# Kernel optimization log

Hardware: AMD Instinct MI355X
Metric: run time of the kernel (lower is better)

## Reference

```python
import jax, jax.numpy as jnp
import numpy as np

B, N, DIM = 4, 2048, 1024
HEADS, DIM_HEAD = 16, 64
INNER = HEADS * DIM_HEAD  # 1024
SCALE = DIM_HEAD ** -0.5

def setup_inputs() -> dict:
    key = jax.random.key(0)
    k1, k2, k3 = jax.random.split(key, 3)
    x = jax.random.normal(k1, (B, N, DIM), dtype=jnp.float32)
    w_qkv = jax.random.normal(k2, (DIM, 3 * INNER), dtype=jnp.float32) * (DIM ** -0.5)
    w_out = jax.random.normal(k3, (INNER, DIM), dtype=jnp.float32) * (INNER ** -0.5)
    b_out = jnp.zeros((DIM,), dtype=jnp.float32)
    return {"x": x, "w_qkv": w_qkv, "w_out": w_out, "b_out": b_out}

def reference(x, w_qkv, w_out, b_out):
    b, n, _ = x.shape
    qkv = x @ w_qkv  # [b, n, 3*inner]
    q, k, v = jnp.split(qkv, 3, axis=-1)
    # [b, n, h, d] -> [b, h, n, d]
    reshape = lambda t: t.reshape(b, n, HEADS, DIM_HEAD).transpose(0, 2, 1, 3)
    q, k, v = reshape(q), reshape(k), reshape(v)
    dots = jnp.einsum('bhqd,bhkd->bhqk', q, k) * SCALE
    attn = jax.nn.softmax(dots, axis=-1)
    out = jnp.einsum('bhqk,bhkd->bhqd', attn, v)
    out = out.transpose(0, 2, 1, 3).reshape(b, n, INNER)
    return out @ w_out + b_out
```

## Files before the change

### kernel.cpp

```cpp
#include <hip/hip_runtime.h>

typedef unsigned short u16;
typedef __bf16 bf16_t;
typedef bf16_t bf16x8 __attribute__((ext_vector_type(8)));
typedef float f32x4 __attribute__((ext_vector_type(4)));
typedef float f32x16 __attribute__((ext_vector_type(16)));
typedef u16 u16x8 __attribute__((ext_vector_type(8)));
typedef u16 u16x4 __attribute__((ext_vector_type(4)));
typedef unsigned uint2v __attribute__((ext_vector_type(2)));

#define B_     4
#define N_     2048
#define DIM_   1024
#define HEADS_ 16
#define DH_    64
#define INNER_ 1024
#define QKV3_  3072
#define SCALE_ 0.125f
#define LOG2E_ 1.44269504089f

__device__ __forceinline__ u16 f2bf(float f) {
  union { float f; unsigned u; } v; v.f = f;
  unsigned r = v.u + 0x7FFFu + ((v.u >> 16) & 1u);
  return (u16)(r >> 16);
}
__device__ __forceinline__ u16 bfbits(float f) {
  bf16_t b = (bf16_t)f;
  return __builtin_bit_cast(u16, b);
}
__device__ __forceinline__ unsigned packbf(float lo, float hi) {
  return (unsigned)bfbits(lo) | ((unsigned)bfbits(hi) << 16);
}

#if __has_builtin(__builtin_amdgcn_exp2f)
#define EXP2F(x) __builtin_amdgcn_exp2f(x)
#else
#define EXP2F(x) __expf((x) * 0.69314718056f)
#endif

typedef __attribute__((address_space(1))) const unsigned int ga_u32;
typedef __attribute__((address_space(3))) unsigned int ls_u32;
__device__ __forceinline__ void gload16(const void* g, void* l) {
  __builtin_amdgcn_global_load_lds((ga_u32*)g, (ls_u32*)l, 16, 0, 0);
}

__global__ __launch_bounds__(256) void cvt_f32_bf16(const float* __restrict__ in,
                                                    u16* __restrict__ out, int n8) {
  int i = blockIdx.x * 256 + threadIdx.x;
  if (i < n8) {
    const float4* p = (const float4*)(in + (size_t)i * 8);
    float4 a = p[0], b = p[1];
    u16x8 o;
    o[0] = f2bf(a.x); o[1] = f2bf(a.y); o[2] = f2bf(a.z); o[3] = f2bf(a.w);
    o[4] = f2bf(b.x); o[5] = f2bf(b.y); o[6] = f2bf(b.z); o[7] = f2bf(b.w);
    *(u16x8*)(out + (size_t)i * 8) = o;
  }
}

__global__ __launch_bounds__(256) void transp_w(const float* __restrict__ in,
                                                u16* __restrict__ out, int Kd, int Nd) {
  __shared__ float t[32][33];
  int n0 = blockIdx.x * 32, k0 = blockIdx.y * 32;
  int tx = threadIdx.x & 31, ty = threadIdx.x >> 5;
#pragma unroll
  for (int i = 0; i < 4; i++)
    t[ty + i * 8][tx] = in[(size_t)(k0 + ty + i * 8) * Nd + n0 + tx];
  __syncthreads();
#pragma unroll
  for (int i = 0; i < 4; i++)
    out[(size_t)(n0 + ty + i * 8) * Kd + k0 + tx] = f2bf(t[tx][ty + i * 8]);
}

__global__ __launch_bounds__(256) void gemm_qkv(const u16* __restrict__ A,
                                                const u16* __restrict__ BT,
                                                u16* __restrict__ qbuf,
                                                u16* __restrict__ ktiled,
                                                u16* __restrict__ vtiled,
                                                int M, int N, int K) {
  __shared__ alignas(16) u16 ldsA[2][128 * 64];
  __shared__ alignas(16) u16 ldsB[2][128 * 64];
  const int tid = threadIdx.x;
  const int lane = tid & 63, wid = tid >> 6;
  const int l16 = lane & 15, lg = lane >> 4;

  int bid = blockIdx.x;
  const int cpx = gridDim.x >> 3;
  bid = (bid & 7) * cpx + (bid >> 3);

  const int ntiles = N >> 7;
  const int tm = bid / ntiles, tn = bid % ntiles;
  const int m0 = tm << 7, n0 = tn << 7;
  const int wr = wid >> 1, wc = wid & 1;

  const int srow_in = lane >> 3;
  const int soff = ((lane & 7) ^ srow_in) * 8;

  f32x4 acc[4][4];
#pragma unroll
  for (int i = 0; i < 4; i++)
#pragma unroll
    for (int j = 0; j < 4; j++) acc[i][j] = f32x4{0.f, 0.f, 0.f, 0.f};

  const int KSTEPS = K >> 6;

#define GSTAGE_(kk, buf)                                                           \
  do {                                                                             \
    const int k1_ = (kk) << 6;                                                     \
    char* bA_ = (char*)&ldsA[(buf)][0];                                            \
    char* bB_ = (char*)&ldsB[(buf)][0];                                            \
    _Pragma("unroll")                                                              \
    for (int i_ = 0; i_ < 4; i_++) {                                               \
      const int rb_ = wid * 32 + i_ * 8;                                           \
      gload16(A  + (size_t)(m0 + rb_ + srow_in) * K + k1_ + soff, bA_ + rb_ * 128);\
      gload16(BT + (size_t)(n0 + rb_ + srow_in) * K + k1_ + soff, bB_ + rb_ * 128);\
    }                                                                              \
  } while (0)

  GSTAGE_(0, 0);
  GSTAGE_(1, 1);

  for (int ks = 0; ks < KSTEPS; ks++) {
    if (ks + 1 < KSTEPS) asm volatile("s_waitcnt vmcnt(8)" ::: "memory");
    else                 asm volatile("s_waitcnt vmcnt(0)" ::: "memory");
    __builtin_amdgcn_s_barrier();

    const char* cA = (const char*)&ldsA[ks & 1][0];
    const char* cB = (const char*)&ldsB[ks & 1][0];

    bf16x8 bf[4][2];
#pragma unroll
    for (int n = 0; n < 4; n++) {
      int row = wc * 64 + n * 16 + l16;
      int rb = row * 128, swz = (row & 7) << 4;
      bf[n][0] = *(const bf16x8*)(cB + rb + ((lg * 16) ^ swz));
      bf[n][1] = *(const bf16x8*)(cB + rb + ((64 + lg * 16) ^ swz));
    }
    __builtin_amdgcn_s_setprio(1);
#pragma unroll
    for (int mm = 0; mm < 4; mm++) {
      int row = wr * 64 + mm * 16 + l16;
      int rb = row * 128, swz = (row & 7) << 4;
      bf16x8 af0 = *(const bf16x8*)(cA + rb + ((lg * 16) ^ swz));
      bf16x8 af1 = *(const bf16x8*)(cA + rb + ((64 + lg * 16) ^ swz));
#pragma unroll
      for (int n = 0; n < 4; n++) {
        acc[mm][n] = __builtin_amdgcn_mfma_f32_16x16x32_bf16(af0, bf[n][0], acc[mm][n], 0, 0, 0);
        acc[mm][n] = __builtin_amdgcn_mfma_f32_16x16x32_bf16(af1, bf[n][1], acc[mm][n], 0, 0, 0);
      }
    }
    __builtin_amdgcn_s_setprio(0);

    __builtin_amdgcn_s_barrier();
    if (ks + 2 < KSTEPS) GSTAGE_(ks + 2, ks & 1);
  }
#undef GSTAGE_

  const int seg = n0 >> 10;
#pragma unroll
  for (int mm = 0; mm < 4; mm++) {
#pragma unroll
    for (int nn = 0; nn < 4; nn++) {
      const int row = m0 + wr * 64 + mm * 16 + lg * 4;
      const int col = n0 + wc * 64 + nn * 16 + l16;
      if (seg == 0) {
#pragma unroll
        for (int j = 0; j < 4; j++)
          qbuf[(size_t)(row + j) * INNER_ + col] = f2bf(acc[mm][nn][j]);
      } else if (seg == 1) {
        const int kd = col - 1024;
        const int h = kd >> 6, s = (kd >> 3) & 7, e = kd & 7;
#pragma unroll
        for (int j = 0; j < 4; j++) {
          const int rr = row + j;
          const int b = rr >> 11, n = rr & (N_ - 1);
          ktiled[(((size_t)(b * HEADS_ + h) * 32 + (n >> 6)) << 12) +
                 (s << 9) + ((n & 63) << 3) + e] = f2bf(acc[mm][nn][j]);
        }
      } else {
        const int vd = col - 2048;
        const int h = vd >> 6, d = vd & 63;
#pragma unroll
        for (int j = 0; j < 4; j++) {
          const int rr = row + j;
          const int b = rr >> 11, n = rr & (N_ - 1);
          vtiled[(((size_t)(b * HEADS_ + h) * 32 + (n >> 6)) << 12) +
                 (((n >> 3) & 7) << 9) + (d << 3) + (n & 7)] = f2bf(acc[mm][nn][j]);
        }
      }
    }
  }
}

__global__ __launch_bounds__(256) void gemm_bt(const u16* __restrict__ A,
                                               const u16* __restrict__ BT,
                                               float* __restrict__ Cp,
                                               const float* __restrict__ bias,
                                               int M, int N, int K) {
  __shared__ alignas(16) u16 ldsA[2][128 * 64];
  __shared__ alignas(16) u16 ldsB[2][128 * 64];
  const int tid = threadIdx.x;
  const int lane = tid & 63, wid = tid >> 6;
  const int l16 = lane & 15, lg = lane >> 4;

  int bid = blockIdx.x;
  const int cpx = gridDim.x >> 3;
  bid = (bid & 7) * cpx + (bid >> 3);

  const int ntiles = N >> 7;
  const int tm = bid / ntiles, tn = bid % ntiles;
  const int m0 = tm << 7, n0 = tn << 7;
  const int wr = wid >> 1, wc = wid & 1;

  const int srow_in = lane >> 3;
  const int soff = ((lane & 7) ^ srow_in) * 8;

  f32x4 acc[4][4];
#pragma unroll
  for (int i = 0; i < 4; i++)
#pragma unroll
    for (int j = 0; j < 4; j++) acc[i][j] = f32x4{0.f, 0.f, 0.f, 0.f};

  const int KSTEPS = K >> 6;

#define GSTAGE_(kk, buf)                                                           \
  do {                                                                             \
    const int k1_ = (kk) << 6;                                                     \
    char* bA_ = (char*)&ldsA[(buf)][0];                                            \
    char* bB_ = (char*)&ldsB[(buf)][0];                                            \
    _Pragma("unroll")                                                              \
    for (int i_ = 0; i_ < 4; i_++) {                                               \
      const int rb_ = wid * 32 + i_ * 8;                                           \
      gload16(A  + (size_t)(m0 + rb_ + srow_in) * K + k1_ + soff, bA_ + rb_ * 128);\
      gload16(BT + (size_t)(n0 + rb_ + srow_in) * K + k1_ + soff, bB_ + rb_ * 128);\
    }                                                                              \
  } while (0)

  GSTAGE_(0, 0);
  GSTAGE_(1, 1);

  for (int ks = 0; ks < KSTEPS; ks++) {
    if (ks + 1 < KSTEPS) asm volatile("s_waitcnt vmcnt(8)" ::: "memory");
    else                 asm volatile("s_waitcnt vmcnt(0)" ::: "memory");
    __builtin_amdgcn_s_barrier();

    const char* cA = (const char*)&ldsA[ks & 1][0];
    const char* cB = (const char*)&ldsB[ks & 1][0];

    bf16x8 bf[4][2];
#pragma unroll
    for (int n = 0; n < 4; n++) {
      int row = wc * 64 + n * 16 + l16;
      int rb = row * 128, swz = (row & 7) << 4;
      bf[n][0] = *(const bf16x8*)(cB + rb + ((lg * 16) ^ swz));
      bf[n][1] = *(const bf16x8*)(cB + rb + ((64 + lg * 16) ^ swz));
    }
    __builtin_amdgcn_s_setprio(1);
#pragma unroll
    for (int mm = 0; mm < 4; mm++) {
      int row = wr * 64 + mm * 16 + l16;
      int rb = row * 128, swz = (row & 7) << 4;
      bf16x8 af0 = *(const bf16x8*)(cA + rb + ((lg * 16) ^ swz));
      bf16x8 af1 = *(const bf16x8*)(cA + rb + ((64 + lg * 16) ^ swz));
#pragma unroll
      for (int n = 0; n < 4; n++) {
        acc[mm][n] = __builtin_amdgcn_mfma_f32_16x16x32_bf16(af0, bf[n][0], acc[mm][n], 0, 0, 0);
        acc[mm][n] = __builtin_amdgcn_mfma_f32_16x16x32_bf16(af1, bf[n][1], acc[mm][n], 0, 0, 0);
      }
    }
    __builtin_amdgcn_s_setprio(0);

    __builtin_amdgcn_s_barrier();
    if (ks + 2 < KSTEPS) GSTAGE_(ks + 2, ks & 1);
  }
#undef GSTAGE_

#pragma unroll
  for (int mm = 0; mm < 4; mm++) {
#pragma unroll
    for (int n = 0; n < 4; n++) {
      int row = m0 + wr * 64 + mm * 16 + lg * 4;
      int col = n0 + wc * 64 + n * 16 + l16;
#pragma unroll
      for (int j = 0; j < 4; j++)
        Cp[(size_t)(row + j) * N + col] = acc[mm][n][j] + bias[col];
    }
  }
}

__global__ __launch_bounds__(512, 4) void attn_fwd(const u16* __restrict__ qbuf,
                                                   const u16* __restrict__ ktiled,
                                                   const u16* __restrict__ vtiled,
                                                   u16* __restrict__ abuf) {
  const int tid = threadIdx.x;
  const int lane = tid & 63, wid = tid >> 6;
  const int l32 = lane & 31, hl = lane >> 5;

  int bid = blockIdx.x;
  bid = (bid & 7) * 64 + (bid >> 3);
  const int bh = bid >> 3, qt = bid & 7;
  const int b = bh >> 4, h = bh & 15;
  const int q0 = qt * 256 + wid * 32;

  constexpr float QS = SCALE_ * LOG2E_;
  bf16x8 qf[4];
  {
    const u16* qrow = qbuf + (size_t)(b * N_ + q0 + l32) * INNER_ + h * DH_ + hl * 8;
#pragma unroll
    for (int step = 0; step < 4; step++) {
      bf16x8 t = *(const bf16x8*)(qrow + step * 16);
#pragma unroll
      for (int i = 0; i < 8; i++) t[i] = (bf16_t)((float)t[i] * QS);
      qf[step] = t;
    }
  }

  const char* kbase = (const char*)(ktiled + (size_t)bh * 131072);
  const char* vbase = (const char*)(vtiled + (size_t)bh * 131072);
  const int kofs = (hl << 10) + (l32 << 4);

  float lrow = 0.f;
  f32x16 acc[2];
#pragma unroll
  for (int i = 0; i < 16; i++) { acc[0][i] = 0.f; acc[1][i] = 0.f; }

  const int NT = N_ / 64;
  for (int kt = 0; kt < NT; ++kt) {
    const char* Kb = kbase + kt * 8192;
    const char* Vb = vbase + kt * 8192;

    f32x16 s[2];
    __builtin_amdgcn_s_setprio(1);
#pragma unroll
    for (int ktile = 0; ktile < 2; ktile++) {
      f32x16 c;
#pragma unroll
      for (int i = 0; i < 16; i++) c[i] = 0.f;
      const char* rb = Kb + (ktile << 9) + kofs;
#pragma unroll
      for (int step = 0; step < 4; step++) {
        bf16x8 kf = *(const bf16x8*)(rb + (step << 11));
        c = __builtin_amdgcn_mfma_f32_32x32x16_bf16(kf, qf[step], c, 0, 0, 0);
      }
      s[ktile] = c;
    }
    __builtin_amdgcn_s_setprio(0);

    float ps0 = 0.f, ps1 = 0.f;
#pragma unroll
    for (int ktile = 0; ktile < 2; ktile++)
#pragma unroll
      for (int i = 0; i < 16; i += 2) {
        const float p0 = EXP2F(s[ktile][i]);
        const float p1 = EXP2F(s[ktile][i + 1]);
        s[ktile][i] = p0; s[ktile][i + 1] = p1;
        ps0 += p0; ps1 += p1;
      }
    lrow += ps0 + ps1;

    bf16x8 pb[4];
#pragma unroll
    for (int ktile = 0; ktile < 2; ktile++)
#pragma unroll
      for (int par = 0; par < 2; par++) {
        const int rb8 = par * 8;
        const unsigned c0 = packbf(s[ktile][rb8 + 0], s[ktile][rb8 + 1]);
        const unsigned c1 = packbf(s[ktile][rb8 + 2], s[ktile][rb8 + 3]);
        const unsigned c2 = packbf(s[ktile][rb8 + 4], s[ktile][rb8 + 5]);
        const unsigned c3 = packbf(s[ktile][rb8 + 6], s[ktile][rb8 + 7]);
        const uint2v r02 = __builtin_amdgcn_permlane32_swap(c0, c2, false, false);
        const uint2v r13 = __builtin_amdgcn_permlane32_swap(c1, c3, false, false);
        union { unsigned u[4]; bf16x8 v; } w;
        w.u[0] = r02[0]; w.u[1] = r13[0]; w.u[2] = r02[1]; w.u[3] = r13[1];
        pb[ktile * 2 + par] = w.v;
      }

    __builtin_amdgcn_s_setprio(1);
#pragma unroll
    for (int dtile = 0; dtile < 2; dtile++) {
      const char* rb = Vb + (dtile << 9) + kofs;
      f32x16 c = acc[dtile];
#pragma unroll
      for (int step = 0; step < 4; step++) {
        bf16x8 vf = *(const bf16x8*)(rb + (step << 11));
        c = __builtin_amdgcn_mfma_f32_32x32x16_bf16(vf, pb[step], c, 0, 0, 0);
      }
      acc[dtile] = c;
    }
    __builtin_amdgcn_s_setprio(0);
  }

  lrow += __shfl_xor(lrow, 32);
  const float inv = 1.f / lrow;
  const size_t row = (size_t)(b * N_ + q0 + l32);
#pragma unroll
  for (int dtile = 0; dtile < 2; dtile++)
#pragma unroll
    for (int g = 0; g < 4; g++) {
      u16x4 w;
#pragma unroll
      for (int j = 0; j < 4; j++) w[j] = bfbits(acc[dtile][g * 4 + j] * inv);
      const int d = dtile * 32 + g * 8 + hl * 4;
      *(u16x4*)(abuf + row * INNER_ + h * DH_ + d) = w;
    }
}

extern "C" void kernel_launch(void* const* d_in, const int* in_sizes, int n_in,
                              void* d_out, int out_size, void* d_ws, size_t ws_size,
                              hipStream_t stream) {
  const float* x     = (const float*)d_in[0];
  const float* w_qkv = (const float*)d_in[1];
  const float* w_out = (const float*)d_in[2];
  const float* b_out = (const float*)d_in[3];
  float* out = (float*)d_out;

  char* ws = (char*)d_ws;
  u16* xb     = (u16*)(ws);
  u16* wqkvT  = (u16*)(ws + (size_t)(16 << 20));
  u16* woutT  = (u16*)(ws + (size_t)(22 << 20));
  u16* qbuf   = (u16*)(ws + (size_t)(24 << 20));
  u16* ktiled = (u16*)(ws + (size_t)(40 << 20));
  u16* vtiled = (u16*)(ws + (size_t)(56 << 20));
  u16* abuf   = xb;

  cvt_f32_bf16<<<4096, 256, 0, stream>>>(x, xb, (B_ * N_ * DIM_) / 8);
  transp_w<<<dim3(QKV3_ / 32, DIM_ / 32), 256, 0, stream>>>(w_qkv, wqkvT, DIM_, QKV3_);
  transp_w<<<dim3(DIM_ / 32, INNER_ / 32), 256, 0, stream>>>(w_out, woutT, INNER_, DIM_);
  gemm_qkv<<<(B_ * N_ / 128) * (QKV3_ / 128), 256, 0, stream>>>(
      xb, wqkvT, qbuf, ktiled, vtiled, B_ * N_, QKV3_, DIM_);
  attn_fwd<<<512, 512, 0, stream>>>(qbuf, ktiled, vtiled, abuf);
  gemm_bt<<<(B_ * N_ / 128) * (DIM_ / 128), 256, 0, stream>>>(
      abuf, woutT, out, b_out, B_ * N_, DIM_, INNER_);
}
```

Before: 212.6 us.

## Stage K/V tiles through double-buffered LDS in attention kernel

The attention kernel now copies each 64-key K and V tile into shared memory with async global-to-LDS loads, double-buffered so the next tile's load overlaps compute on the current one. Before, every wave read K/V fragments straight from global memory. Blocks shrink to 256 threads covering 128 queries, and the grid grows to 1024 with a new XCD-aware block mapping. This cuts duplicate global/L2 traffic across the waves of a block, at the cost of a barrier every tile and 32KB of LDS per block.

```diff
diff --git a/kernel.cpp b/kernel.cpp
--- a/kernel.cpp
+++ b/kernel.cpp
@@ -287,19 +287,23 @@
   }
 }
 
-__global__ __launch_bounds__(512, 4) void attn_fwd(const u16* __restrict__ qbuf,
+__global__ __launch_bounds__(256, 5) void attn_fwd(const u16* __restrict__ qbuf,
                                                    const u16* __restrict__ ktiled,
                                                    const u16* __restrict__ vtiled,
                                                    u16* __restrict__ abuf) {
+  __shared__ alignas(16) u16 ldsK[2][4096];
+  __shared__ alignas(16) u16 ldsV[2][4096];
+
   const int tid = threadIdx.x;
   const int lane = tid & 63, wid = tid >> 6;
   const int l32 = lane & 31, hl = lane >> 5;
 
-  int bid = blockIdx.x;
-  bid = (bid & 7) * 64 + (bid >> 3);
-  const int bh = bid >> 3, qt = bid & 7;
+  const int i = blockIdx.x;
+  const int t = i >> 3, xcd = i & 7;
+  const int bh = xcd * 8 + (t >> 4);
+  const int qt = t & 15;
   const int b = bh >> 4, h = bh & 15;
-  const int q0 = qt * 256 + wid * 32;
+  const int q0 = qt * 128 + wid * 32;
 
   constexpr float QS = SCALE_ * LOG2E_;
   bf16x8 qf[4];
@@ -307,26 +311,43 @@
     const u16* qrow = qbuf + (size_t)(b * N_ + q0 + l32) * INNER_ + h * DH_ + hl * 8;
 #pragma unroll
     for (int step = 0; step < 4; step++) {
-      bf16x8 t = *(const bf16x8*)(qrow + step * 16);
-#pragma unroll
-      for (int i = 0; i < 8; i++) t[i] = (bf16_t)((float)t[i] * QS);
-      qf[step] = t;
-    }
-  }
-
-  const char* kbase = (const char*)(ktiled + (size_t)bh * 131072);
-  const char* vbase = (const char*)(vtiled + (size_t)bh * 131072);
+      bf16x8 t2 = *(const bf16x8*)(qrow + step * 16);
+#pragma unroll
+      for (int ii = 0; ii < 8; ii++) t2[ii] = (bf16_t)((float)t2[ii] * QS);
+      qf[step] = t2;
+    }
+  }
+
+  const u16* kts = ktiled + (size_t)bh * 131072 + wid * 512 + lane * 8;
+  const u16* vts = vtiled + (size_t)bh * 131072 + wid * 512 + lane * 8;
+  const int sdst = wid << 10;
+
+#define STAGE_(tt, buf)                                                     \
+  do {                                                                      \
+    gload16(kts + (size_t)(tt) * 4096,        (char*)ldsK + (buf) * 8192 + sdst);        \
+    gload16(kts + (size_t)(tt) * 4096 + 2048, (char*)ldsK + (buf) * 8192 + 4096 + sdst); \
+    gload16(vts + (size_t)(tt) * 4096,        (char*)ldsV + (buf) * 8192 + sdst);        \
+    gload16(vts + (size_t)(tt) * 4096 + 2048, (char*)ldsV + (buf) * 8192 + 4096 + sdst); \
+  } while (0)
+
   const int kofs = (hl << 10) + (l32 << 4);
 
   float lrow = 0.f;
   f32x16 acc[2];
 #pragma unroll
-  for (int i = 0; i < 16; i++) { acc[0][i] = 0.f; acc[1][i] = 0.f; }
+  for (int ii = 0; ii < 16; ii++) { acc[0][ii] = 0.f; acc[1][ii] = 0.f; }
+
+  STAGE_(0, 0);
 
   const int NT = N_ / 64;
   for (int kt = 0; kt < NT; ++kt) {
-    const char* Kb = kbase + kt * 8192;
-    const char* Vb = vbase + kt * 8192;
+    const int cur = kt & 1;
+    asm volatile("s_waitcnt vmcnt(0)" ::: "memory");
+    __builtin_amdgcn_s_barrier();
+    if (kt + 1 < NT) STAGE_(kt + 1, cur ^ 1);
+
+    const char* Kb = (const char*)ldsK + cur * 8192;
+    const char* Vb = (const char*)ldsV + cur * 8192;
 
     f32x16 s[2];
     __builtin_amdgcn_s_setprio(1);
@@ -334,7 +355,7 @@
     for (int ktile = 0; ktile < 2; ktile++) {
       f32x16 c;
 #pragma unroll
-      for (int i = 0; i < 16; i++) c[i] = 0.f;
+      for (int ii = 0; ii < 16; ii++) c[ii] = 0.f;
       const char* rb = Kb + (ktile << 9) + kofs;
 #pragma unroll
       for (int step = 0; step < 4; step++) {
@@ -349,10 +370,10 @@
 #pragma unroll
     for (int ktile = 0; ktile < 2; ktile++)
 #pragma unroll
-      for (int i = 0; i < 16; i += 2) {
-        const float p0 = EXP2F(s[ktile][i]);
-        const float p1 = EXP2F(s[ktile][i + 1]);
-        s[ktile][i] = p0; s[ktile][i + 1] = p1;
+      for (int ii = 0; ii < 16; ii += 2) {
+        const float p0 = EXP2F(s[ktile][ii]);
+        const float p1 = EXP2F(s[ktile][ii + 1]);
+        s[ktile][ii] = p0; s[ktile][ii + 1] = p1;
         ps0 += p0; ps1 += p1;
       }
     lrow += ps0 + ps1;
@@ -388,6 +409,7 @@
     }
     __builtin_amdgcn_s_setprio(0);
   }
+#undef STAGE_
 
   lrow += __shfl_xor(lrow, 32);
   const float inv = 1.f / lrow;
@@ -427,7 +449,7 @@
   transp_w<<<dim3(DIM_ / 32, INNER_ / 32), 256, 0, stream>>>(w_out, woutT, INNER_, DIM_);
   gemm_qkv<<<(B_ * N_ / 128) * (QKV3_ / 128), 256, 0, stream>>>(
       xb, wqkvT, qbuf, ktiled, vtiled, B_ * N_, QKV3_, DIM_);
-  attn_fwd<<<512, 512, 0, stream>>>(qbuf, ktiled, vtiled, abuf);
+  attn_fwd<<<1024, 256, 0, stream>>>(qbuf, ktiled, vtiled, abuf);
   gemm_bt<<<(B_ * N_ / 128) * (DIM_ / 128), 256, 0, stream>>>(
       abuf, woutT, out, b_out, B_ * N_, DIM_, INNER_);
 }
```

Measured after the change: 198.6 us. -6.6%, faster.
